# Kernel tuning notes

Hardware: AMD Instinct MI355X
Metric: run time of the kernel (lower is better)

## Reference

```python
import jax, jax.numpy as jnp
import numpy as np

DIM = 64
OUT_DIM = 64
CUTOFF = 5.0
N = 2048


def setup_inputs() -> dict:
    key = jax.random.key(0)
    k_atoms, k_w = jax.random.split(key)
    atoms = jax.random.normal(k_atoms, (N, 3), dtype=jnp.float32) * 5.0
    init = jax.nn.initializers.glorot_normal()
    # Original code (buggily) reuses the same key for both inits; we mirror that.
    w1 = init(k_w, (DIM, 4), jnp.float32)
    w2 = init(k_w, (4, OUT_DIM), jnp.float32)
    return {"atoms": atoms, "w1": w1, "w2": w2, "n_atoms": N}


def reference(atoms, w1, w2, n_atoms):
    # f_k = (k+1) * pi, k = 0..dim-1
    f = (jnp.arange(DIM, dtype=jnp.float32) + 1.0) * jnp.pi
    # pairwise distances: (N, N)
    diff = atoms[None, :, :] - atoms[:, None, :]
    x = jnp.linalg.norm(diff, axis=-1)
    x_ext = x[..., None] + 1e-08                     # (N, N, 1)
    # Bessel RBF basis: (N, N, dim)
    basis = jnp.sqrt(2.0 / CUTOFF) * jnp.sin(f * x_ext / CUTOFF) / x_ext
    # tiny projection dim -> 4 -> out_dim; contract small dim first
    w = w1 @ w2                                      # (dim, out_dim)
    return jnp.einsum('ijd,do->ijo', basis, w)
```

## Files before the change

### kernel.cpp

```cpp
#include <hip/hip_runtime.h>
#include <math.h>

#define NATOMS 2048
#define DIM 64

typedef float f32x4 __attribute__((ext_vector_type(4)));


template <int CTRL>
__device__ __forceinline__ float dpp_add(float v) {
    int m = __builtin_amdgcn_update_dpp(0, __float_as_int(v), CTRL, 0xF, 0xF, true);
    return v + __int_as_float(m);
}
__device__ __forceinline__ float swz_add_xor4(float v) {
    return v + __int_as_float(__builtin_amdgcn_ds_swizzle(__float_as_int(v), 0x101F));
}

__global__ __launch_bounds__(256) void bessel_rbf_kernel(
    const float* __restrict__ atoms,
    const float* __restrict__ w1,
    const float* __restrict__ w2,
    float* __restrict__ out)
{
    const int lane = threadIdx.x & 63;
    const int waveInBlock = threadIdx.x >> 6;
    const int q = lane & 7;
    const int g = lane >> 3;
    const int d0 = q * 8;

    float w1r[8][4];
#pragma unroll
    for (int k = 0; k < 8; ++k) {
        float4 v = *reinterpret_cast<const float4*>(w1 + (d0 + k) * 4);
        w1r[k][0] = v.x; w1r[k][1] = v.y; w1r[k][2] = v.z; w1r[k][3] = v.w;
    }

    const float PREF = 0.6324555320336759f;
    float w2a[4][4], w2b[4][4];
#pragma unroll
    for (int m = 0; m < 4; ++m) {
        float4 va = *reinterpret_cast<const float4*>(w2 + m * DIM + 4 * q);
        float4 vb = *reinterpret_cast<const float4*>(w2 + m * DIM + 32 + 4 * q);
        w2a[m][0] = va.x * PREF; w2a[m][1] = va.y * PREF;
        w2a[m][2] = va.z * PREF; w2a[m][3] = va.w * PREF;
        w2b[m][0] = vb.x * PREF; w2b[m][1] = vb.y * PREF;
        w2b[m][2] = vb.z * PREF; w2b[m][3] = vb.w * PREF;
    }

    const unsigned totalPairs = (unsigned)NATOMS * (unsigned)NATOMS;
    const unsigned wavesTotal = (unsigned)gridDim.x * (blockDim.x >> 6);
    const unsigned wid = (unsigned)blockIdx.x * (blockDim.x >> 6) + waveInBlock;

    const float dk1 = (float)(d0 + 1);

    f32x4* __restrict__ out4 = reinterpret_cast<f32x4*>(out);

#pragma unroll 1
    for (unsigned p0 = wid * 8; p0 < totalPairs; p0 += wavesTotal * 8) {
        const int i = __builtin_amdgcn_readfirstlane((int)(p0 >> 11));
        const int j = (int)(p0 & (NATOMS - 1)) + g;

        const float ax = atoms[i * 3 + 0];
        const float ay = atoms[i * 3 + 1];
        const float az = atoms[i * 3 + 2];
        const float bx = atoms[j * 3 + 0];
        const float by = atoms[j * 3 + 1];
        const float bz = atoms[j * 3 + 2];

        const float dx = ax - bx, dy = ay - by, dz = az - bz;
        float x = __builtin_amdgcn_sqrtf(fmaf(dx, dx, fmaf(dy, dy, dz * dz)));
        x += 1e-8f;
        const float inv = __builtin_amdgcn_rcpf(x);
        const float xr  = x * 0.1f;

        float r0 = dk1 * xr;
        float r1 = r0 + xr;
        r0 = r0 - floorf(r0);
        r1 = r1 - floorf(r1);
        float rc = xr - floorf(xr);
        const float a0   = __builtin_amdgcn_sinf(r0) * inv;
        const float a1   = __builtin_amdgcn_sinf(r1) * inv;
        const float c1   = __builtin_amdgcn_cosf(rc);
        const float twoC = c1 + c1;

        float t[4];
#pragma unroll
        for (int m = 0; m < 4; ++m)
            t[m] = fmaf(a1, w1r[1][m], a0 * w1r[0][m]);
        float sp = a0, sc = a1;
#pragma unroll
        for (int k = 2; k < 8; ++k) {
            const float sn = fmaf(twoC, sc, -sp);
#pragma unroll
            for (int m = 0; m < 4; ++m)
                t[m] = fmaf(sn, w1r[k][m], t[m]);
            sp = sc; sc = sn;
        }

#pragma unroll
        for (int m = 0; m < 4; ++m) {
            t[m] = dpp_add<0xB1>(t[m]);
            t[m] = dpp_add<0x4E>(t[m]);
            t[m] = swz_add_xor4(t[m]);
        }

        f32x4 oA, oB;
        oA.x = fmaf(t[0], w2a[0][0], fmaf(t[1], w2a[1][0], fmaf(t[2], w2a[2][0], t[3] * w2a[3][0])));
        oA.y = fmaf(t[0], w2a[0][1], fmaf(t[1], w2a[1][1], fmaf(t[2], w2a[2][1], t[3] * w2a[3][1])));
        oA.z = fmaf(t[0], w2a[0][2], fmaf(t[1], w2a[1][2], fmaf(t[2], w2a[2][2], t[3] * w2a[3][2])));
        oA.w = fmaf(t[0], w2a[0][3], fmaf(t[1], w2a[1][3], fmaf(t[2], w2a[2][3], t[3] * w2a[3][3])));
        oB.x = fmaf(t[0], w2b[0][0], fmaf(t[1], w2b[1][0], fmaf(t[2], w2b[2][0], t[3] * w2b[3][0])));
        oB.y = fmaf(t[0], w2b[0][1], fmaf(t[1], w2b[1][1], fmaf(t[2], w2b[2][1], t[3] * w2b[3][1])));
        oB.z = fmaf(t[0], w2b[0][2], fmaf(t[1], w2b[1][2], fmaf(t[2], w2b[2][2], t[3] * w2b[3][2])));
        oB.w = fmaf(t[0], w2b[0][3], fmaf(t[1], w2b[1][3], fmaf(t[2], w2b[2][3], t[3] * w2b[3][3])));

        const size_t base = (size_t)(p0 + (unsigned)g) * 16;
        __builtin_nontemporal_store(oA, &out4[base + q]);
        __builtin_nontemporal_store(oB, &out4[base + 8 + q]);
    }
}

extern "C" void kernel_launch(void* const* d_in, const int* in_sizes, int n_in,
                              void* d_out, int out_size, void* d_ws, size_t ws_size,
                              hipStream_t stream) {
    const float* atoms = (const float*)d_in[0];
    const float* w1    = (const float*)d_in[1];
    const float* w2    = (const float*)d_in[2];
    float* out         = (float*)d_out;

    dim3 grid(2048), block(256);
    hipLaunchKernelGGL(bessel_rbf_kernel, grid, block, 0, stream, atoms, w1, w2, out);
}
```

Measured before the change: 220.3 us.

## Stage atoms in LDS and give each wave a contiguous row segment

Each block now copies all atom coordinates into shared memory, and atom loads in the loop read from LDS instead of global memory. The work split changes from a grid-strided pair loop to a fixed 512-column segment of one row per wave, so the i-atom load is hoisted out of the loop. Output stores switch from nontemporal to regular stores. The cost is a 24KB LDS fill and a barrier in every block, and LDS use may limit occupancy.

```diff
diff --git a/kernel.cpp b/kernel.cpp
--- a/kernel.cpp
+++ b/kernel.cpp
@@ -22,11 +22,22 @@
     const float* __restrict__ w2,
     float* __restrict__ out)
 {
-    const int lane = threadIdx.x & 63;
-    const int waveInBlock = threadIdx.x >> 6;
+    __shared__ float s_at[NATOMS * 3];
+
+    const int tid  = threadIdx.x;
+    const int lane = tid & 63;
+    const int waveInBlock = tid >> 6;
     const int q = lane & 7;
     const int g = lane >> 3;
     const int d0 = q * 8;
+
+    {
+        const float4* ga = reinterpret_cast<const float4*>(atoms);
+        float4* sa = reinterpret_cast<float4*>(s_at);
+#pragma unroll
+        for (int r = 0; r < 6; ++r)
+            sa[tid + 256 * r] = ga[tid + 256 * r];
+    }
 
     float w1r[8][4];
 #pragma unroll
@@ -34,7 +45,6 @@
         float4 v = *reinterpret_cast<const float4*>(w1 + (d0 + k) * 4);
         w1r[k][0] = v.x; w1r[k][1] = v.y; w1r[k][2] = v.z; w1r[k][3] = v.w;
     }
-
     const float PREF = 0.6324555320336759f;
     float w2a[4][4], w2b[4][4];
 #pragma unroll
@@ -47,25 +57,28 @@
         w2b[m][2] = vb.z * PREF; w2b[m][3] = vb.w * PREF;
     }
 
-    const unsigned totalPairs = (unsigned)NATOMS * (unsigned)NATOMS;
-    const unsigned wavesTotal = (unsigned)gridDim.x * (blockDim.x >> 6);
-    const unsigned wid = (unsigned)blockIdx.x * (blockDim.x >> 6) + waveInBlock;
+    __syncthreads();
+
+    const unsigned wid = __builtin_amdgcn_readfirstlane(
+        (unsigned)blockIdx.x * 4u + (unsigned)waveInBlock);
+    const int i       = (int)(wid >> 2);
+    const int colBase = (int)(wid & 3u) * 512;
+
+    const float ax = s_at[i * 3 + 0];
+    const float ay = s_at[i * 3 + 1];
+    const float az = s_at[i * 3 + 2];
 
     const float dk1 = (float)(d0 + 1);
-
     f32x4* __restrict__ out4 = reinterpret_cast<f32x4*>(out);
+    const size_t rowBase = (size_t)i * 2048 + (size_t)colBase;
 
 #pragma unroll 1
-    for (unsigned p0 = wid * 8; p0 < totalPairs; p0 += wavesTotal * 8) {
-        const int i = __builtin_amdgcn_readfirstlane((int)(p0 >> 11));
-        const int j = (int)(p0 & (NATOMS - 1)) + g;
+    for (int it = 0; it < 64; ++it) {
+        const int j = colBase + it * 8 + g;
 
-        const float ax = atoms[i * 3 + 0];
-        const float ay = atoms[i * 3 + 1];
-        const float az = atoms[i * 3 + 2];
-        const float bx = atoms[j * 3 + 0];
-        const float by = atoms[j * 3 + 1];
-        const float bz = atoms[j * 3 + 2];
+        const float bx = s_at[j * 3 + 0];
+        const float by = s_at[j * 3 + 1];
+        const float bz = s_at[j * 3 + 2];
 
         const float dx = ax - bx, dy = ay - by, dz = az - bz;
         float x = __builtin_amdgcn_sqrtf(fmaf(dx, dx, fmaf(dy, dy, dz * dz)));
@@ -114,9 +127,9 @@
         oB.z = fmaf(t[0], w2b[0][2], fmaf(t[1], w2b[1][2], fmaf(t[2], w2b[2][2], t[3] * w2b[3][2])));
         oB.w = fmaf(t[0], w2b[0][3], fmaf(t[1], w2b[1][3], fmaf(t[2], w2b[2][3], t[3] * w2b[3][3])));
 
-        const size_t base = (size_t)(p0 + (unsigned)g) * 16;
-        __builtin_nontemporal_store(oA, &out4[base + q]);
-        __builtin_nontemporal_store(oB, &out4[base + 8 + q]);
+        const size_t base = (rowBase + (size_t)(it * 8 + g)) * 16;
+        out4[base + q]     = oA;
+        out4[base + 8 + q] = oB;
     }
 }
 
```

Result: faster. 200.3 us (-9.1%).

## Tile pairs by row/column block with LDS-staged atoms and 16-lane pair groups

Applied to the files above, without the earlier changes.

Each block now handles 4 rows and a 256-column tile. The column atoms are staged in shared memory, and each wave loops 64 times over fixed pairs instead of a grid-stride loop. Each pair is now spread over 16 lanes with 4 basis dims each, so the reduction becomes four DPP row ops instead of DPP plus ds_swizzle. The output store shrinks to one 16-byte store per lane, and that store is no longer nontemporal. This cuts global atom loads and cross-lane swizzle cost, but doubles the transcendental work per pair and adds a launch-bounds occupancy hint.

```diff
diff --git a/kernel.cpp b/kernel.cpp
--- a/kernel.cpp
+++ b/kernel.cpp
@@ -12,60 +12,64 @@
     int m = __builtin_amdgcn_update_dpp(0, __float_as_int(v), CTRL, 0xF, 0xF, true);
     return v + __int_as_float(m);
 }
-__device__ __forceinline__ float swz_add_xor4(float v) {
-    return v + __int_as_float(__builtin_amdgcn_ds_swizzle(__float_as_int(v), 0x101F));
-}
 
-__global__ __launch_bounds__(256) void bessel_rbf_kernel(
+__global__ __launch_bounds__(256, 6) void bessel_rbf_kernel(
     const float* __restrict__ atoms,
     const float* __restrict__ w1,
     const float* __restrict__ w2,
     float* __restrict__ out)
 {
-    const int lane = threadIdx.x & 63;
-    const int waveInBlock = threadIdx.x >> 6;
-    const int q = lane & 7;
-    const int g = lane >> 3;
-    const int d0 = q * 8;
+    __shared__ float s_at[256 * 3];
 
-    float w1r[8][4];
+    const int tid  = threadIdx.x;
+    const int lane = tid & 63;
+    const int waveInBlock = tid >> 6;
+    const int q = lane & 15;
+    const int g = lane >> 4;
+    const int d0 = q * 4;
+
+    const int w        = (int)(blockIdx.x & 7u);
+    const int rowGroup = (int)(blockIdx.x >> 3);
+    const int i        = rowGroup * 4 + waveInBlock;
+    const int colBase  = w * 256;
+
+    if (tid < 192) {
+        reinterpret_cast<float4*>(s_at)[tid] =
+            reinterpret_cast<const float4*>(atoms)[w * 192 + tid];
+    }
+
+    float w1r[4][4];
 #pragma unroll
-    for (int k = 0; k < 8; ++k) {
+    for (int k = 0; k < 4; ++k) {
         float4 v = *reinterpret_cast<const float4*>(w1 + (d0 + k) * 4);
         w1r[k][0] = v.x; w1r[k][1] = v.y; w1r[k][2] = v.z; w1r[k][3] = v.w;
     }
-
     const float PREF = 0.6324555320336759f;
-    float w2a[4][4], w2b[4][4];
+    float w2c[4][4];
 #pragma unroll
     for (int m = 0; m < 4; ++m) {
-        float4 va = *reinterpret_cast<const float4*>(w2 + m * DIM + 4 * q);
-        float4 vb = *reinterpret_cast<const float4*>(w2 + m * DIM + 32 + 4 * q);
-        w2a[m][0] = va.x * PREF; w2a[m][1] = va.y * PREF;
-        w2a[m][2] = va.z * PREF; w2a[m][3] = va.w * PREF;
-        w2b[m][0] = vb.x * PREF; w2b[m][1] = vb.y * PREF;
-        w2b[m][2] = vb.z * PREF; w2b[m][3] = vb.w * PREF;
+        float4 v = *reinterpret_cast<const float4*>(w2 + m * DIM + 4 * q);
+        w2c[m][0] = v.x * PREF; w2c[m][1] = v.y * PREF;
+        w2c[m][2] = v.z * PREF; w2c[m][3] = v.w * PREF;
     }
 
-    const unsigned totalPairs = (unsigned)NATOMS * (unsigned)NATOMS;
-    const unsigned wavesTotal = (unsigned)gridDim.x * (blockDim.x >> 6);
-    const unsigned wid = (unsigned)blockIdx.x * (blockDim.x >> 6) + waveInBlock;
+    const float ax = atoms[i * 3 + 0];
+    const float ay = atoms[i * 3 + 1];
+    const float az = atoms[i * 3 + 2];
+
+    __syncthreads();
 
     const float dk1 = (float)(d0 + 1);
-
     f32x4* __restrict__ out4 = reinterpret_cast<f32x4*>(out);
+    const unsigned pairBase = (unsigned)i * 2048u + (unsigned)colBase;
 
 #pragma unroll 1
-    for (unsigned p0 = wid * 8; p0 < totalPairs; p0 += wavesTotal * 8) {
-        const int i = __builtin_amdgcn_readfirstlane((int)(p0 >> 11));
-        const int j = (int)(p0 & (NATOMS - 1)) + g;
+    for (int it = 0; it < 64; ++it) {
+        const int jl = it * 4 + g;
 
-        const float ax = atoms[i * 3 + 0];
-        const float ay = atoms[i * 3 + 1];
-        const float az = atoms[i * 3 + 2];
-        const float bx = atoms[j * 3 + 0];
-        const float by = atoms[j * 3 + 1];
-        const float bz = atoms[j * 3 + 2];
+        const float bx = s_at[jl * 3 + 0];
+        const float by = s_at[jl * 3 + 1];
+        const float bz = s_at[jl * 3 + 2];
 
         const float dx = ax - bx, dy = ay - by, dz = az - bz;
         float x = __builtin_amdgcn_sqrtf(fmaf(dx, dx, fmaf(dy, dy, dz * dz)));
@@ -82,41 +86,32 @@
         const float a1   = __builtin_amdgcn_sinf(r1) * inv;
         const float c1   = __builtin_amdgcn_cosf(rc);
         const float twoC = c1 + c1;
+        const float a2   = fmaf(twoC, a1, -a0);
+        const float a3   = fmaf(twoC, a2, -a1);
 
         float t[4];
 #pragma unroll
-        for (int m = 0; m < 4; ++m)
+        for (int m = 0; m < 4; ++m) {
             t[m] = fmaf(a1, w1r[1][m], a0 * w1r[0][m]);
-        float sp = a0, sc = a1;
-#pragma unroll
-        for (int k = 2; k < 8; ++k) {
-            const float sn = fmaf(twoC, sc, -sp);
-#pragma unroll
-            for (int m = 0; m < 4; ++m)
-                t[m] = fmaf(sn, w1r[k][m], t[m]);
-            sp = sc; sc = sn;
+            t[m] = fmaf(a2, w1r[2][m], t[m]);
+            t[m] = fmaf(a3, w1r[3][m], t[m]);
         }
 
 #pragma unroll
         for (int m = 0; m < 4; ++m) {
-            t[m] = dpp_add<0xB1>(t[m]);
-            t[m] = dpp_add<0x4E>(t[m]);
-            t[m] = swz_add_xor4(t[m]);
+            t[m] = dpp_add<0x128>(t[m]);
+            t[m] = dpp_add<0x124>(t[m]);
+            t[m] = dpp_add<0x122>(t[m]);
+            t[m] = dpp_add<0x121>(t[m]);
         }
 
-        f32x4 oA, oB;
-        oA.x = fmaf(t[0], w2a[0][0], fmaf(t[1], w2a[1][0], fmaf(t[2], w2a[2][0], t[3] * w2a[3][0])));
-        oA.y = fmaf(t[0], w2a[0][1], fmaf(t[1], w2a[1][1], fmaf(t[2], w2a[2][1], t[3] * w2a[3][1])));
-        oA.z = fmaf(t[0], w2a[0][2], fmaf(t[1], w2a[1][2], fmaf(t[2], w2a[2][2], t[3] * w2a[3][2])));
-        oA.w = fmaf(t[0], w2a[0][3], fmaf(t[1], w2a[1][3], fmaf(t[2], w2a[2][3], t[3] * w2a[3][3])));
-        oB.x = fmaf(t[0], w2b[0][0], fmaf(t[1], w2b[1][0], fmaf(t[2], w2b[2][0], t[3] * w2b[3][0])));
-        oB.y = fmaf(t[0], w2b[0][1], fmaf(t[1], w2b[1][1], fmaf(t[2], w2b[2][1], t[3] * w2b[3][1])));
-        oB.z = fmaf(t[0], w2b[0][2], fmaf(t[1], w2b[1][2], fmaf(t[2], w2b[2][2], t[3] * w2b[3][2])));
-        oB.w = fmaf(t[0], w2b[0][3], fmaf(t[1], w2b[1][3], fmaf(t[2], w2b[2][3], t[3] * w2b[3][3])));
+        f32x4 o4;
+        o4.x = fmaf(t[0], w2c[0][0], fmaf(t[1], w2c[1][0], fmaf(t[2], w2c[2][0], t[3] * w2c[3][0])));
+        o4.y = fmaf(t[0], w2c[0][1], fmaf(t[1], w2c[1][1], fmaf(t[2], w2c[2][1], t[3] * w2c[3][1])));
+        o4.z = fmaf(t[0], w2c[0][2], fmaf(t[1], w2c[1][2], fmaf(t[2], w2c[2][2], t[3] * w2c[3][2])));
+        o4.w = fmaf(t[0], w2c[0][3], fmaf(t[1], w2c[1][3], fmaf(t[2], w2c[2][3], t[3] * w2c[3][3])));
 
-        const size_t base = (size_t)(p0 + (unsigned)g) * 16;
-        __builtin_nontemporal_store(oA, &out4[base + q]);
-        __builtin_nontemporal_store(oB, &out4[base + 8 + q]);
+        out4[(pairBase + (unsigned)jl) * 16u + (unsigned)q] = o4;
     }
 }
 
@@ -128,6 +123,6 @@
     const float* w2    = (const float*)d_in[2];
     float* out         = (float*)d_out;
 
-    dim3 grid(2048), block(256);
+    dim3 grid(4096), block(256);
     hipLaunchKernelGGL(bessel_rbf_kernel, grid, block, 0, stream, atoms, w1, w2, out);
 }
```

New measurement: 208.1 us. -5.6%, faster.
